# Kernel tuning notes

Hardware: AMD Instinct MI355X
Metric: run time of the kernel (lower is better)

## Reference

```python
import jax, jax.numpy as jnp
import numpy as np

EPS = 1e-08


def setup_inputs() -> dict:
    key = jax.random.key(0)
    k1, k2 = jax.random.split(key)
    N, D, C = 8192, 512, 1000
    features = jax.random.uniform(k1, (N, D), dtype=jnp.float32)
    logits = jax.random.normal(k2, (N, C), dtype=jnp.float32)
    return {"features": features, "logits": logits}


def reference(features, logits):
    N = features.shape[0]
    # softmax over classes, plus eps (matches F.softmax(...) + eps)
    p = jax.nn.softmax(logits, axis=1) + EPS                     # [N, C]
    # similarity matrix with diagonal removed
    cos_sim = features @ features.T - jnp.eye(N, dtype=features.dtype)  # [N, N]
    neighbor_mask = (cos_sim >= -1).astype(cos_sim.dtype)
    w = cos_sim * neighbor_mask
    w = w / jnp.sum(w, axis=1, keepdims=True)                    # row-normalized weights
    weighted_sum_nb = w @ p                                      # [N, C]
    # F.kl_div(log_input, target, reduction='batchmean')
    # = sum(target * (log(target) - log_input)) / N
    kl = jnp.sum(weighted_sum_nb * (jnp.log(weighted_sum_nb) - jnp.log(p))) / N
    return kl
```

## Files before the change

### kernel.cpp

```cpp
#include <hip/hip_runtime.h>
#include <math.h>

#define NN 8192
#define DD 512
#define CC 1000
#define CP 1024

typedef __attribute__((ext_vector_type(8))) short short8;
typedef __attribute__((ext_vector_type(4))) float f32x4;
typedef __attribute__((ext_vector_type(4))) unsigned short us4;
typedef __attribute__((ext_vector_type(8))) unsigned short us8;
typedef __attribute__((ext_vector_type(4))) unsigned int ui4;

__device__ __forceinline__ float bf2f(unsigned short u){
  union{unsigned int i; float f;} v; v.i = ((unsigned int)u)<<16; return v.f;
}
__device__ __forceinline__ unsigned short f2bf(float f){
  union{float f; unsigned int i;} v; v.f = f;
  unsigned int r = v.i + 0x7FFF + ((v.i>>16)&1);
  return (unsigned short)(r>>16);
}
__device__ __forceinline__ float waveRedSum(float v){
  #pragma unroll
  for(int o=32;o;o>>=1) v += __shfl_xor(v,o,64);
  return v;
}
__device__ __forceinline__ float waveRedMax(float v){
  #pragma unroll
  for(int o=32;o;o>>=1) v = fmaxf(v,__shfl_xor(v,o,64));
  return v;
}
__device__ __forceinline__ void gload_lds16(const void* g, void* l){
  __builtin_amdgcn_global_load_lds((const __attribute__((address_space(1))) void*)g,
                                   (__attribute__((address_space(3))) void*)l, 16, 0, 0);
}

__global__ __launch_bounds__(256) void k_prep(const float* __restrict__ F,
                                              const float* __restrict__ L,
                                              unsigned short* __restrict__ FbT,
                                              unsigned short* __restrict__ Fb,
                                              float* __restrict__ gpart,
                                              unsigned short* __restrict__ PbT){
  __shared__ __align__(16) char smem[8*1028*4];
  int bid = blockIdx.x;
  int grp = bid/3, r = bid - grp*3;
  int t = threadIdx.x;

  if(r < 2){
    int cb = grp*2 + r;
    unsigned short* lds = (unsigned short*)smem;
    float* gq = (float*)(smem + 64*68*2);
    int i0 = (cb & 127)*64, d0 = (cb >> 7)*64;
    int cx = t&15, ry = t>>4;
    float ca0=0.f,ca1=0.f,ca2=0.f,ca3=0.f;
    #pragma unroll
    for(int rr=0;rr<4;rr++){
      int row = rr*16 + ry;
      f32x4 fv = *(const f32x4*)&F[(size_t)(i0+row)*DD + d0 + cx*4];
      us4 u; u[0]=f2bf(fv[0]); u[1]=f2bf(fv[1]); u[2]=f2bf(fv[2]); u[3]=f2bf(fv[3]);
      *(us4*)&lds[row*68 + cx*4] = u;
      *(us4*)&Fb[(size_t)(i0+row)*DD + d0 + cx*4] = u;
      ca0+=fv[0]; ca1+=fv[1]; ca2+=fv[2]; ca3+=fv[3];
    }
    {
      f32x4 cv; cv[0]=ca0; cv[1]=ca1; cv[2]=ca2; cv[3]=ca3;
      *(f32x4*)&gq[ry*64 + cx*4] = cv;
    }
    __syncthreads();
    #pragma unroll
    for(int rr=0;rr<4;rr++){
      int d = rr*16 + ry;
      us4 u;
      #pragma unroll
      for(int q=0;q<4;q++) u[q] = lds[(cx*4+q)*68 + d];
      *(us4*)&FbT[(size_t)(d0+d)*NN + i0 + cx*4] = u;
    }
    __syncthreads();
    if(t<64){
      float s=0.f;
      #pragma unroll
      for(int j=0;j<16;j++) s += gq[j*64+t];
      gpart[cb&127 ? (cb&127)*DD + d0 + t : d0 + t] = s;
    }
  } else {
    int sb = grp;
    unsigned int (*lt)[1028] = (unsigned int(*)[1028])smem;
    int l = t&63, w = t>>6;
    int i0 = sb*16;
    #pragma unroll
    for(int q=0;q<4;q++){
      int rr = w*4 + q;
      int row = i0 + rr;
      const float* lr = L + (size_t)row*CC;
      float v[16]; float mx = -1e30f;
      #pragma unroll
      for(int k=0;k<16;k++){ int c = l + 64*k; v[k] = (c<CC)? lr[c] : -1e30f; mx = fmaxf(mx,v[k]); }
      mx = waveRedMax(mx);
      float s = 0.f;
      #pragma unroll
      for(int k=0;k<16;k++){ v[k] = __expf(v[k]-mx); s += v[k]; }
      s = waveRedSum(s);
      float inv = 1.0f/s;
      #pragma unroll
      for(int k=0;k<16;k++){
        int c = l + 64*k;
        float p = v[k]*inv + 1e-8f;
        unsigned short h = (c<CC)? f2bf(p) : (unsigned short)0;
        *((unsigned short*)&lt[rr>>1][c] + (rr&1)) = h;
      }
    }
    __syncthreads();
    #pragma unroll
    for(int k=0;k<4;k++){
      int c = t + 256*k;
      ui4 a, b;
      #pragma unroll
      for(int j=0;j<4;j++){ a[j] = lt[j][c]; b[j] = lt[j+4][c]; }
      *(ui4*)&PbT[(size_t)c*NN + i0]     = a;
      *(ui4*)&PbT[(size_t)c*NN + i0 + 8] = b;
    }
  }
}

__global__ __launch_bounds__(256,2) void k_gemm1(const unsigned short* __restrict__ A,
                                                 const unsigned short* __restrict__ B,
                                                 unsigned short* __restrict__ Tpb,
                                                 const float* __restrict__ gpart,
                                                 float* __restrict__ g){
  __shared__ unsigned short Al[128*64];
  __shared__ unsigned short Bl[128*64];
  __shared__ float rs[4][64];
  int bid = blockIdx.x;
  int t = threadIdx.x;
  if(bid >= 512){
    int gb = bid - 512;
    int d = gb*64 + (t&63);
    int q = t>>6;
    float s = 0.f;
    #pragma unroll
    for(int j=0;j<32;j++) s += gpart[(size_t)(q*32+j)*DD + d];
    rs[q][t&63] = s;
    __syncthreads();
    if(q==0) g[d] = rs[0][t&63]+rs[1][t&63]+rs[2][t&63]+rs[3][t&63];
    return;
  }
  int l = t&63, w = t>>6;
  int bx = bid & 7, byz = bid >> 3;
  int by = byz & 3, bz = byz >> 2;
  int m0 = bx*128, n0 = by*128;
  int k0 = bz*512;
  int wm = w>>1, wn = w&1;
  f32x4 acc[4][4] = {};
  int srow = w*32 + (l>>3);
  int scl  = (l&7) ^ (srow&7);
  const unsigned short* Ab = A + (size_t)(m0 + srow)*NN + k0 + scl*8;
  const unsigned short* Bb = B + (size_t)(n0 + srow)*NN + k0 + scl*8;
  unsigned short* AlB = Al + (w*32)*64;
  unsigned short* BlB = Bl + (w*32)*64;

  for(int kt=0; kt<512; kt+=64){
    __syncthreads();
    #pragma unroll
    for(int q=0;q<4;q++){
      gload_lds16(Ab + (size_t)q*8*NN + kt, AlB + q*8*64);
      gload_lds16(Bb + (size_t)q*8*NN + kt, BlB + q*8*64);
    }
    asm volatile("s_waitcnt vmcnt(0)" ::: "memory");
    __syncthreads();
    #pragma unroll
    for(int ks=0;ks<2;ks++){
      short8 af[4], bf[4];
      #pragma unroll
      for(int mi=0;mi<4;mi++){
        int rr = wm*64 + mi*16 + (l&15);
        int ch = ((ks<<2) + (l>>4)) ^ (rr&7);
        af[mi] = *(const short8*)&Al[rr*64 + ch*8];
      }
      #pragma unroll
      for(int ni=0;ni<4;ni++){
        int rr = wn*64 + ni*16 + (l&15);
        int ch = ((ks<<2) + (l>>4)) ^ (rr&7);
        bf[ni] = *(const short8*)&Bl[rr*64 + ch*8];
      }
      #pragma unroll
      for(int mi=0;mi<4;mi++)
        #pragma unroll
        for(int ni=0;ni<4;ni++)
          acc[mi][ni] = __builtin_amdgcn_mfma_f32_16x16x32_bf16(af[mi], bf[ni], acc[mi][ni], 0,0,0);
    }
  }
  unsigned short* Tz = Tpb + (size_t)bz*CP*DD;
  int rbase = (l>>4)*4;
  #pragma unroll
  for(int mi=0;mi<4;mi++){
    int c = m0 + wm*64 + mi*16 + rbase;
    #pragma unroll
    for(int ni=0;ni<4;ni++){
      int d = n0 + wn*64 + ni*16 + (l&15);
      #pragma unroll
      for(int j=0;j<4;j++)
        Tz[(size_t)(c+j)*DD + d] = f2bf(acc[mi][ni][j]);
    }
  }
}

__global__ __launch_bounds__(256) void k_redT(const unsigned short* __restrict__ Tpb,
                                              const unsigned short* __restrict__ Fb,
                                              const float* __restrict__ g,
                                              unsigned short* __restrict__ Ttb,
                                              float* __restrict__ invr){
  int t = threadIdx.x;
  size_t i = ((size_t)blockIdx.x*256 + (size_t)t)*8;
  f32x4 s0 = {0.f,0.f,0.f,0.f}, s1 = {0.f,0.f,0.f,0.f};
  #pragma unroll
  for(int z=0;z<16;z++){
    us8 v = *(const us8*)&Tpb[(size_t)z*CP*DD + i];
    s0[0]+=bf2f(v[0]); s0[1]+=bf2f(v[1]); s0[2]+=bf2f(v[2]); s0[3]+=bf2f(v[3]);
    s1[0]+=bf2f(v[4]); s1[1]+=bf2f(v[5]); s1[2]+=bf2f(v[6]); s1[3]+=bf2f(v[7]);
  }
  us8 u;
  u[0]=f2bf(s0[0]); u[1]=f2bf(s0[1]); u[2]=f2bf(s0[2]); u[3]=f2bf(s0[3]);
  u[4]=f2bf(s1[0]); u[5]=f2bf(s1[1]); u[6]=f2bf(s1[2]); u[7]=f2bf(s1[3]);
  *(us8*)&Ttb[i] = u;
  int row = blockIdx.x*32 + (t>>3);
  int seg = (t&7)*64;
  const unsigned short* fr = Fb + (size_t)row*DD + seg;
  const float* gr = g + seg;
  float s = 0.f;
  #pragma unroll
  for(int j=0;j<8;j++){
    us8 f8 = *(const us8*)&fr[j*8];
    f32x4 ga = *(const f32x4*)&gr[j*8];
    f32x4 gb = *(const f32x4*)&gr[j*8+4];
    s += bf2f(f8[0])*ga[0]+bf2f(f8[1])*ga[1]+bf2f(f8[2])*ga[2]+bf2f(f8[3])*ga[3]
       + bf2f(f8[4])*gb[0]+bf2f(f8[5])*gb[1]+bf2f(f8[6])*gb[2]+bf2f(f8[7])*gb[3];
  }
  s += __shfl_xor(s,1,64); s += __shfl_xor(s,2,64); s += __shfl_xor(s,4,64);
  if((t&7)==0) invr[row] = 1.0f/(s - 1.0f);
}

__global__ __launch_bounds__(256,2) void k_gemm2(const unsigned short* __restrict__ Fb,
                                                 const unsigned short* __restrict__ Bt,
                                                 const unsigned short* __restrict__ PbT,
                                                 const float* __restrict__ invr,
                                                 float* __restrict__ partials){
  __shared__ unsigned short Al[128*64];
  __shared__ unsigned short Bl[128*64];
  __shared__ float red[4];
  int t = threadIdx.x, l = t&63, w = t>>6;
  int m0 = blockIdx.y*128, n0 = blockIdx.x*128;
  int wm = w>>1, wn = w&1;
  f32x4 acc[4][4] = {};
  int srow = w*32 + (l>>3);
  int scl  = (l&7) ^ (srow&7);
  const unsigned short* Ab = Fb + (size_t)(m0 + srow)*DD + scl*8;
  const unsigned short* Bb = Bt + (size_t)(n0 + srow)*DD + scl*8;
  unsigned short* AlB = Al + (w*32)*64;
  unsigned short* BlB = Bl + (w*32)*64;

  for(int kt=0; kt<512; kt+=64){
    __syncthreads();
    #pragma unroll
    for(int q=0;q<4;q++){
      gload_lds16(Ab + (size_t)q*8*DD + kt, AlB + q*8*64);
      gload_lds16(Bb + (size_t)q*8*DD + kt, BlB + q*8*64);
    }
    asm volatile("s_waitcnt vmcnt(0)" ::: "memory");
    __syncthreads();
    #pragma unroll
    for(int ks=0;ks<2;ks++){
      short8 af[4], bf[4];
      #pragma unroll
      for(int mi=0;mi<4;mi++){
        int rr = wm*64 + mi*16 + (l&15);
        int ch = ((ks<<2) + (l>>4)) ^ (rr&7);
        af[mi] = *(const short8*)&Al[rr*64 + ch*8];
      }
      #pragma unroll
      for(int ni=0;ni<4;ni++){
        int rr = wn*64 + ni*16 + (l&15);
        int ch = ((ks<<2) + (l>>4)) ^ (rr&7);
        bf[ni] = *(const short8*)&Bl[rr*64 + ch*8];
      }
      #pragma unroll
      for(int mi=0;mi<4;mi++)
        #pragma unroll
        for(int ni=0;ni<4;ni++)
          acc[mi][ni] = __builtin_amdgcn_mfma_f32_16x16x32_bf16(af[mi], bf[ni], acc[mi][ni], 0,0,0);
    }
  }
  float kl = 0.f;
  int rbase = (l>>4)*4;
  #pragma unroll
  for(int mi=0;mi<4;mi++){
    int i_base = m0 + wm*64 + mi*16 + rbase;
    f32x4 ir4 = *(const f32x4*)&invr[i_base];
    #pragma unroll
    for(int ni=0;ni<4;ni++){
      int c = n0 + wn*64 + ni*16 + (l&15);
      if(c < CC){
        us4 p4 = *(const us4*)&PbT[(size_t)c*NN + i_base];
        #pragma unroll
        for(int j=0;j<4;j++){
          float p = bf2f(p4[j]);
          float ws = (acc[mi][ni][j] - p) * ir4[j];
          kl += ws * (__logf(ws) - __logf(p));
        }
      }
    }
  }
  kl = waveRedSum(kl);
  if(l==0) red[w]=kl;
  __syncthreads();
  if(t==0) partials[blockIdx.y*8 + blockIdx.x] = red[0]+red[1]+red[2]+red[3];
}

__global__ __launch_bounds__(64) void k_finalize(const float* __restrict__ partials,
                                                 float* __restrict__ out){
  int l = threadIdx.x;
  double s = 0.0;
  for(int j=l; j<512; j+=64) s += (double)partials[j];
  #pragma unroll
  for(int o=32;o;o>>=1) s += __shfl_xor(s,o,64);
  if(l==0) out[0] = (float)(s / (double)NN);
}

extern "C" void kernel_launch(void* const* d_in, const int* in_sizes, int n_in,
                              void* d_out, int out_size, void* d_ws, size_t ws_size,
                              hipStream_t stream){
  const float* F = (const float*)d_in[0];
  const float* L = (const float*)d_in[1];
  float* out = (float*)d_out;

  unsigned char* w8 = (unsigned char*)d_ws;
  unsigned short* FbT = (unsigned short*)w8;
  unsigned short* PbT = (unsigned short*)(w8 + (8u<<20));
  unsigned short* Tpb = (unsigned short*)(w8 + (24u<<20));
  unsigned short* Ttb = (unsigned short*)(w8 + (40u<<20));
  unsigned short* Fb  = (unsigned short*)(w8 + (41u<<20));
  float* gpart        = (float*)(w8 + (49u<<20));
  float* g            = (float*)(w8 + (49u<<20) + 262144);
  float* invr         = (float*)(w8 + (49u<<20) + 264192);
  float* partials     = (float*)(w8 + (49u<<20) + 296960);

  hipLaunchKernelGGL(k_prep,     dim3(1536),   dim3(256), 0, stream, F, L, FbT, Fb, gpart, PbT);
  hipLaunchKernelGGL(k_gemm1,    dim3(520),    dim3(256), 0, stream, PbT, FbT, Tpb, gpart, g);
  hipLaunchKernelGGL(k_redT,     dim3(256),    dim3(256), 0, stream, Tpb, Fb, g, Ttb, invr);
  hipLaunchKernelGGL(k_gemm2,    dim3(8,64),   dim3(256), 0, stream, Fb, Ttb, PbT, invr, partials);
  hipLaunchKernelGGL(k_finalize, dim3(1),      dim3(64),  0, stream, partials, out);
}
```

Baseline: 73.74 us.

## Fuse gemm1, reduction, gemm2 and finalize into one cooperative kernel with grid syncs

Merges the four post-prep kernels into a single cooperative launch of 512 blocks, separated by grid.sync barriers, with a swizzled block-to-tile mapping. The goal is to remove kernel launch gaps and tail effects between the small stages. The g-reduction moves onto the first 8 GEMM blocks, and the T reduction is re-tiled to 256 threads times 4 elements per block. In exchange it needs all 512 blocks resident at once, and each grid barrier costs time and can serialize work.

```diff
diff --git a/kernel.cpp b/kernel.cpp
--- a/kernel.cpp
+++ b/kernel.cpp
@@ -1,10 +1,14 @@
 #include <hip/hip_runtime.h>
+#include <hip/hip_cooperative_groups.h>
 #include <math.h>
+
+namespace cg = cooperative_groups;
 
 #define NN 8192
 #define DD 512
 #define CC 1000
 #define CP 1024
+#define CPD (CP*DD)
 
 typedef __attribute__((ext_vector_type(8))) short short8;
 typedef __attribute__((ext_vector_type(4))) float f32x4;
@@ -80,7 +84,7 @@
       float s=0.f;
       #pragma unroll
       for(int j=0;j<16;j++) s += gq[j*64+t];
-      gpart[cb&127 ? (cb&127)*DD + d0 + t : d0 + t] = s;
+      gpart[(cb&127)*DD + d0 + t] = s;
     }
   } else {
     int sb = grp;
@@ -122,207 +126,198 @@
   }
 }
 
-__global__ __launch_bounds__(256,2) void k_gemm1(const unsigned short* __restrict__ A,
-                                                 const unsigned short* __restrict__ B,
-                                                 unsigned short* __restrict__ Tpb,
-                                                 const float* __restrict__ gpart,
-                                                 float* __restrict__ g){
-  __shared__ unsigned short Al[128*64];
-  __shared__ unsigned short Bl[128*64];
+__global__ __launch_bounds__(256,2) void k_main(const unsigned short* __restrict__ PbT,
+                                                const unsigned short* __restrict__ FbT,
+                                                unsigned short* __restrict__ Tpb,
+                                                const float* __restrict__ gpart,
+                                                float* __restrict__ g,
+                                                const unsigned short* __restrict__ Fb,
+                                                unsigned short* __restrict__ Ttb,
+                                                float* __restrict__ invr,
+                                                float* __restrict__ partials,
+                                                float* __restrict__ out){
+  cg::grid_group grid = cg::this_grid();
+  __shared__ __align__(16) unsigned short Al[128*64];
+  __shared__ __align__(16) unsigned short Bl[128*64];
   __shared__ float rs[4][64];
+  __shared__ float red[4];
   int bid = blockIdx.x;
-  int t = threadIdx.x;
-  if(bid >= 512){
-    int gb = bid - 512;
-    int d = gb*64 + (t&63);
-    int q = t>>6;
-    float s = 0.f;
-    #pragma unroll
-    for(int j=0;j<32;j++) s += gpart[(size_t)(q*32+j)*DD + d];
-    rs[q][t&63] = s;
-    __syncthreads();
-    if(q==0) g[d] = rs[0][t&63]+rs[1][t&63]+rs[2][t&63]+rs[3][t&63];
-    return;
-  }
-  int l = t&63, w = t>>6;
-  int bx = bid & 7, byz = bid >> 3;
-  int by = byz & 3, bz = byz >> 2;
-  int m0 = bx*128, n0 = by*128;
-  int k0 = bz*512;
+  int t = threadIdx.x, l = t&63, w = t>>6;
   int wm = w>>1, wn = w&1;
-  f32x4 acc[4][4] = {};
   int srow = w*32 + (l>>3);
   int scl  = (l&7) ^ (srow&7);
-  const unsigned short* Ab = A + (size_t)(m0 + srow)*NN + k0 + scl*8;
-  const unsigned short* Bb = B + (size_t)(n0 + srow)*NN + k0 + scl*8;
   unsigned short* AlB = Al + (w*32)*64;
   unsigned short* BlB = Bl + (w*32)*64;
-
-  for(int kt=0; kt<512; kt+=64){
-    __syncthreads();
-    #pragma unroll
-    for(int q=0;q<4;q++){
-      gload_lds16(Ab + (size_t)q*8*NN + kt, AlB + q*8*64);
-      gload_lds16(Bb + (size_t)q*8*NN + kt, BlB + q*8*64);
-    }
-    asm volatile("s_waitcnt vmcnt(0)" ::: "memory");
-    __syncthreads();
-    #pragma unroll
-    for(int ks=0;ks<2;ks++){
-      short8 af[4], bf[4];
-      #pragma unroll
-      for(int mi=0;mi<4;mi++){
-        int rr = wm*64 + mi*16 + (l&15);
-        int ch = ((ks<<2) + (l>>4)) ^ (rr&7);
-        af[mi] = *(const short8*)&Al[rr*64 + ch*8];
-      }
+  int Lsw = (bid&7)*64 + (bid>>3);
+
+  {
+    int bx = Lsw&7, by = (Lsw>>3)&3, bz = Lsw>>5;
+    int m0 = bx*128, n0 = by*128, k0 = bz*512;
+    f32x4 acc[4][4] = {};
+    const unsigned short* Ab = PbT + (size_t)(m0 + srow)*NN + k0 + scl*8;
+    const unsigned short* Bb = FbT + (size_t)(n0 + srow)*NN + k0 + scl*8;
+    for(int kt=0; kt<512; kt+=64){
+      __syncthreads();
+      #pragma unroll
+      for(int q=0;q<4;q++){
+        gload_lds16(Ab + (size_t)q*8*NN + kt, AlB + q*8*64);
+        gload_lds16(Bb + (size_t)q*8*NN + kt, BlB + q*8*64);
+      }
+      asm volatile("s_waitcnt vmcnt(0)" ::: "memory");
+      __syncthreads();
+      #pragma unroll
+      for(int ks=0;ks<2;ks++){
+        short8 af[4], bf[4];
+        #pragma unroll
+        for(int mi=0;mi<4;mi++){
+          int rr = wm*64 + mi*16 + (l&15);
+          int ch = ((ks<<2) + (l>>4)) ^ (rr&7);
+          af[mi] = *(const short8*)&Al[rr*64 + ch*8];
+        }
+        #pragma unroll
+        for(int ni=0;ni<4;ni++){
+          int rr = wn*64 + ni*16 + (l&15);
+          int ch = ((ks<<2) + (l>>4)) ^ (rr&7);
+          bf[ni] = *(const short8*)&Bl[rr*64 + ch*8];
+        }
+        #pragma unroll
+        for(int mi=0;mi<4;mi++)
+          #pragma unroll
+          for(int ni=0;ni<4;ni++)
+            acc[mi][ni] = __builtin_amdgcn_mfma_f32_16x16x32_bf16(af[mi], bf[ni], acc[mi][ni], 0,0,0);
+      }
+    }
+    unsigned short* Tz = Tpb + (size_t)bz*CPD;
+    int rbase = (l>>4)*4;
+    #pragma unroll
+    for(int mi=0;mi<4;mi++){
+      int c = m0 + wm*64 + mi*16 + rbase;
       #pragma unroll
       for(int ni=0;ni<4;ni++){
-        int rr = wn*64 + ni*16 + (l&15);
-        int ch = ((ks<<2) + (l>>4)) ^ (rr&7);
-        bf[ni] = *(const short8*)&Bl[rr*64 + ch*8];
-      }
-      #pragma unroll
-      for(int mi=0;mi<4;mi++)
-        #pragma unroll
-        for(int ni=0;ni<4;ni++)
-          acc[mi][ni] = __builtin_amdgcn_mfma_f32_16x16x32_bf16(af[mi], bf[ni], acc[mi][ni], 0,0,0);
-    }
-  }
-  unsigned short* Tz = Tpb + (size_t)bz*CP*DD;
-  int rbase = (l>>4)*4;
-  #pragma unroll
-  for(int mi=0;mi<4;mi++){
-    int c = m0 + wm*64 + mi*16 + rbase;
-    #pragma unroll
-    for(int ni=0;ni<4;ni++){
-      int d = n0 + wn*64 + ni*16 + (l&15);
-      #pragma unroll
-      for(int j=0;j<4;j++)
-        Tz[(size_t)(c+j)*DD + d] = f2bf(acc[mi][ni][j]);
-    }
-  }
-}
-
-__global__ __launch_bounds__(256) void k_redT(const unsigned short* __restrict__ Tpb,
-                                              const unsigned short* __restrict__ Fb,
-                                              const float* __restrict__ g,
-                                              unsigned short* __restrict__ Ttb,
-                                              float* __restrict__ invr){
-  int t = threadIdx.x;
-  size_t i = ((size_t)blockIdx.x*256 + (size_t)t)*8;
-  f32x4 s0 = {0.f,0.f,0.f,0.f}, s1 = {0.f,0.f,0.f,0.f};
-  #pragma unroll
-  for(int z=0;z<16;z++){
-    us8 v = *(const us8*)&Tpb[(size_t)z*CP*DD + i];
-    s0[0]+=bf2f(v[0]); s0[1]+=bf2f(v[1]); s0[2]+=bf2f(v[2]); s0[3]+=bf2f(v[3]);
-    s1[0]+=bf2f(v[4]); s1[1]+=bf2f(v[5]); s1[2]+=bf2f(v[6]); s1[3]+=bf2f(v[7]);
-  }
-  us8 u;
-  u[0]=f2bf(s0[0]); u[1]=f2bf(s0[1]); u[2]=f2bf(s0[2]); u[3]=f2bf(s0[3]);
-  u[4]=f2bf(s1[0]); u[5]=f2bf(s1[1]); u[6]=f2bf(s1[2]); u[7]=f2bf(s1[3]);
-  *(us8*)&Ttb[i] = u;
-  int row = blockIdx.x*32 + (t>>3);
-  int seg = (t&7)*64;
-  const unsigned short* fr = Fb + (size_t)row*DD + seg;
-  const float* gr = g + seg;
-  float s = 0.f;
-  #pragma unroll
-  for(int j=0;j<8;j++){
-    us8 f8 = *(const us8*)&fr[j*8];
-    f32x4 ga = *(const f32x4*)&gr[j*8];
-    f32x4 gb = *(const f32x4*)&gr[j*8+4];
-    s += bf2f(f8[0])*ga[0]+bf2f(f8[1])*ga[1]+bf2f(f8[2])*ga[2]+bf2f(f8[3])*ga[3]
-       + bf2f(f8[4])*gb[0]+bf2f(f8[5])*gb[1]+bf2f(f8[6])*gb[2]+bf2f(f8[7])*gb[3];
-  }
-  s += __shfl_xor(s,1,64); s += __shfl_xor(s,2,64); s += __shfl_xor(s,4,64);
-  if((t&7)==0) invr[row] = 1.0f/(s - 1.0f);
-}
-
-__global__ __launch_bounds__(256,2) void k_gemm2(const unsigned short* __restrict__ Fb,
-                                                 const unsigned short* __restrict__ Bt,
-                                                 const unsigned short* __restrict__ PbT,
-                                                 const float* __restrict__ invr,
-                                                 float* __restrict__ partials){
-  __shared__ unsigned short Al[128*64];
-  __shared__ unsigned short Bl[128*64];
-  __shared__ float red[4];
-  int t = threadIdx.x, l = t&63, w = t>>6;
-  int m0 = blockIdx.y*128, n0 = blockIdx.x*128;
-  int wm = w>>1, wn = w&1;
-  f32x4 acc[4][4] = {};
-  int srow = w*32 + (l>>3);
-  int scl  = (l&7) ^ (srow&7);
-  const unsigned short* Ab = Fb + (size_t)(m0 + srow)*DD + scl*8;
-  const unsigned short* Bb = Bt + (size_t)(n0 + srow)*DD + scl*8;
-  unsigned short* AlB = Al + (w*32)*64;
-  unsigned short* BlB = Bl + (w*32)*64;
-
-  for(int kt=0; kt<512; kt+=64){
-    __syncthreads();
-    #pragma unroll
-    for(int q=0;q<4;q++){
-      gload_lds16(Ab + (size_t)q*8*DD + kt, AlB + q*8*64);
-      gload_lds16(Bb + (size_t)q*8*DD + kt, BlB + q*8*64);
-    }
-    asm volatile("s_waitcnt vmcnt(0)" ::: "memory");
-    __syncthreads();
-    #pragma unroll
-    for(int ks=0;ks<2;ks++){
-      short8 af[4], bf[4];
-      #pragma unroll
-      for(int mi=0;mi<4;mi++){
-        int rr = wm*64 + mi*16 + (l&15);
-        int ch = ((ks<<2) + (l>>4)) ^ (rr&7);
-        af[mi] = *(const short8*)&Al[rr*64 + ch*8];
-      }
+        int d = n0 + wn*64 + ni*16 + (l&15);
+        #pragma unroll
+        for(int j=0;j<4;j++)
+          Tz[(size_t)(c+j)*DD + d] = f2bf(acc[mi][ni][j]);
+      }
+    }
+    if(bid < 8){
+      int d = bid*64 + (t&63);
+      int q = t>>6;
+      float s = 0.f;
+      #pragma unroll
+      for(int j=0;j<32;j++) s += gpart[(size_t)(q*32+j)*DD + d];
+      rs[q][t&63] = s;
+      __syncthreads();
+      if(q==0) g[d] = rs[0][t&63]+rs[1][t&63]+rs[2][t&63]+rs[3][t&63];
+    }
+  }
+  grid.sync();
+
+  {
+    size_t i = ((size_t)bid*256 + (size_t)t)*4;
+    f32x4 s0 = {0.f,0.f,0.f,0.f};
+    #pragma unroll
+    for(int z=0;z<16;z++){
+      us4 v = *(const us4*)&Tpb[(size_t)z*CPD + i];
+      s0[0]+=bf2f(v[0]); s0[1]+=bf2f(v[1]); s0[2]+=bf2f(v[2]); s0[3]+=bf2f(v[3]);
+    }
+    us4 u; u[0]=f2bf(s0[0]); u[1]=f2bf(s0[1]); u[2]=f2bf(s0[2]); u[3]=f2bf(s0[3]);
+    *(us4*)&Ttb[i] = u;
+    int row = bid*16 + (t>>4);
+    int seg = (t&15)*32;
+    const unsigned short* fr = Fb + (size_t)row*DD + seg;
+    const float* gr = g + seg;
+    float s = 0.f;
+    #pragma unroll
+    for(int j=0;j<4;j++){
+      us8 f8 = *(const us8*)&fr[j*8];
+      f32x4 ga = *(const f32x4*)&gr[j*8];
+      f32x4 gb = *(const f32x4*)&gr[j*8+4];
+      s += bf2f(f8[0])*ga[0]+bf2f(f8[1])*ga[1]+bf2f(f8[2])*ga[2]+bf2f(f8[3])*ga[3]
+         + bf2f(f8[4])*gb[0]+bf2f(f8[5])*gb[1]+bf2f(f8[6])*gb[2]+bf2f(f8[7])*gb[3];
+    }
+    s += __shfl_xor(s,1,64); s += __shfl_xor(s,2,64);
+    s += __shfl_xor(s,4,64); s += __shfl_xor(s,8,64);
+    if((t&15)==0) invr[row] = 1.0f/(s - 1.0f);
+  }
+  grid.sync();
+
+  {
+    int n0 = (Lsw&7)*128;
+    int m0 = (Lsw>>3)*128;
+    f32x4 acc[4][4] = {};
+    const unsigned short* Ab = Fb + (size_t)(m0 + srow)*DD + scl*8;
+    const unsigned short* Bb = Ttb + (size_t)(n0 + srow)*DD + scl*8;
+    for(int kt=0; kt<512; kt+=64){
+      __syncthreads();
+      #pragma unroll
+      for(int q=0;q<4;q++){
+        gload_lds16(Ab + (size_t)q*8*DD + kt, AlB + q*8*64);
+        gload_lds16(Bb + (size_t)q*8*DD + kt, BlB + q*8*64);
+      }
+      asm volatile("s_waitcnt vmcnt(0)" ::: "memory");
+      __syncthreads();
+      #pragma unroll
+      for(int ks=0;ks<2;ks++){
+        short8 af[4], bf[4];
+        #pragma unroll
+        for(int mi=0;mi<4;mi++){
+          int rr = wm*64 + mi*16 + (l&15);
+          int ch = ((ks<<2) + (l>>4)) ^ (rr&7);
+          af[mi] = *(const short8*)&Al[rr*64 + ch*8];
+        }
+        #pragma unroll
+        for(int ni=0;ni<4;ni++){
+          int rr = wn*64 + ni*16 + (l&15);
+          int ch = ((ks<<2) + (l>>4)) ^ (rr&7);
+          bf[ni] = *(const short8*)&Bl[rr*64 + ch*8];
+        }
+        #pragma unroll
+        for(int mi=0;mi<4;mi++)
+          #pragma unroll
+          for(int ni=0;ni<4;ni++)
+            acc[mi][ni] = __builtin_amdgcn_mfma_f32_16x16x32_bf16(af[mi], bf[ni], acc[mi][ni], 0,0,0);
+      }
+    }
+    float kl = 0.f;
+    int rbase = (l>>4)*4;
+    #pragma unroll
+    for(int mi=0;mi<4;mi++){
+      int i_base = m0 + wm*64 + mi*16 + rbase;
+      f32x4 ir4 = *(const f32x4*)&invr[i_base];
       #pragma unroll
       for(int ni=0;ni<4;ni++){
-        int rr = wn*64 + ni*16 + (l&15);
-        int ch = ((ks<<2) + (l>>4)) ^ (rr&7);
-        bf[ni] = *(const short8*)&Bl[rr*64 + ch*8];
-      }
-      #pragma unroll
-      for(int mi=0;mi<4;mi++)
-        #pragma unroll
-        for(int ni=0;ni<4;ni++)
-          acc[mi][ni] = __builtin_amdgcn_mfma_f32_16x16x32_bf16(af[mi], bf[ni], acc[mi][ni], 0,0,0);
-    }
-  }
-  float kl = 0.f;
-  int rbase = (l>>4)*4;
-  #pragma unroll
-  for(int mi=0;mi<4;mi++){
-    int i_base = m0 + wm*64 + mi*16 + rbase;
-    f32x4 ir4 = *(const f32x4*)&invr[i_base];
-    #pragma unroll
-    for(int ni=0;ni<4;ni++){
-      int c = n0 + wn*64 + ni*16 + (l&15);
-      if(c < CC){
-        us4 p4 = *(const us4*)&PbT[(size_t)c*NN + i_base];
-        #pragma unroll
-        for(int j=0;j<4;j++){
-          float p = bf2f(p4[j]);
-          float ws = (acc[mi][ni][j] - p) * ir4[j];
-          kl += ws * (__logf(ws) - __logf(p));
-        }
-      }
-    }
-  }
-  kl = waveRedSum(kl);
-  if(l==0) red[w]=kl;
-  __syncthreads();
-  if(t==0) partials[blockIdx.y*8 + blockIdx.x] = red[0]+red[1]+red[2]+red[3];
-}
-
-__global__ __launch_bounds__(64) void k_finalize(const float* __restrict__ partials,
-                                                 float* __restrict__ out){
-  int l = threadIdx.x;
-  double s = 0.0;
-  for(int j=l; j<512; j+=64) s += (double)partials[j];
-  #pragma unroll
-  for(int o=32;o;o>>=1) s += __shfl_xor(s,o,64);
-  if(l==0) out[0] = (float)(s / (double)NN);
+        int c = n0 + wn*64 + ni*16 + (l&15);
+        if(c < CC){
+          us4 p4 = *(const us4*)&PbT[(size_t)c*NN + i_base];
+          #pragma unroll
+          for(int j=0;j<4;j++){
+            float p = bf2f(p4[j]);
+            float ws = (acc[mi][ni][j] - p) * ir4[j];
+            kl += ws * (__logf(ws) - __logf(p));
+          }
+        }
+      }
+    }
+    kl = waveRedSum(kl);
+    if(l==0) red[w]=kl;
+    __syncthreads();
+    if(t==0) partials[Lsw] = red[0]+red[1]+red[2]+red[3];
+  }
+  grid.sync();
+
+  if(bid==0){
+    double* ds = (double*)Al;
+    double s = (double)partials[t] + (double)partials[t+256];
+    ds[t] = s;
+    __syncthreads();
+    #pragma unroll
+    for(int o=128;o;o>>=1){
+      if(t<o) ds[t] += ds[t+o];
+      __syncthreads();
+    }
+    if(t==0) out[0] = (float)(ds[0] / (double)NN);
+  }
 }
 
 extern "C" void kernel_launch(void* const* d_in, const int* in_sizes, int n_in,
@@ -343,9 +338,9 @@
   float* invr         = (float*)(w8 + (49u<<20) + 264192);
   float* partials     = (float*)(w8 + (49u<<20) + 296960);
 
-  hipLaunchKernelGGL(k_prep,     dim3(1536),   dim3(256), 0, stream, F, L, FbT, Fb, gpart, PbT);
-  hipLaunchKernelGGL(k_gemm1,    dim3(520),    dim3(256), 0, stream, PbT, FbT, Tpb, gpart, g);
-  hipLaunchKernelGGL(k_redT,     dim3(256),    dim3(256), 0, stream, Tpb, Fb, g, Ttb, invr);
-  hipLaunchKernelGGL(k_gemm2,    dim3(8,64),   dim3(256), 0, stream, Fb, Ttb, PbT, invr, partials);
-  hipLaunchKernelGGL(k_finalize, dim3(1),      dim3(64),  0, stream, partials, out);
-}
+  hipLaunchKernelGGL(k_prep, dim3(1536), dim3(256), 0, stream, F, L, FbT, Fb, gpart, PbT);
+
+  void* args[] = {(void*)&PbT, (void*)&FbT, (void*)&Tpb, (void*)&gpart, (void*)&g,
+                  (void*)&Fb, (void*)&Ttb, (void*)&invr, (void*)&partials, (void*)&out};
+  hipLaunchCooperativeKernel((const void*)k_main, dim3(512), dim3(256), args, 0, stream);
+}
```

Measured after the change: 252.3 us. +242.1%, slower.
